# Performance work log

Hardware: AMD Instinct MI355X
Metric: run time of the kernel (lower is better)

Reference implementation:

```python
import jax, jax.numpy as jnp
import numpy as np

UNITS = 1024
OUT_STEPS = 32
NUM_FEATURES = 4
BATCH = 1024
IN_STEPS = 64


def setup_inputs() -> dict:
    key = jax.random.key(0)
    k = jax.random.split(key, 6)
    x = jax.random.normal(k[0], (BATCH, IN_STEPS, NUM_FEATURES), jnp.float32)
    # Keras LSTMCell params: kernel [F,4u], recurrent_kernel [u,4u], bias [4u]
    W = jax.random.normal(k[1], (NUM_FEATURES, 4 * UNITS), jnp.float32) * 0.3
    U = jax.random.normal(k[2], (UNITS, 4 * UNITS), jnp.float32) * 0.03
    b = jnp.zeros((4 * UNITS,), jnp.float32)
    Wd = jax.random.normal(k[3], (UNITS, NUM_FEATURES), jnp.float32) * 0.05
    bd = jnp.zeros((NUM_FEATURES,), jnp.float32)
    return {"x": x, "W": W, "U": U, "b": b, "Wd": Wd, "bd": bd}


def _lstm_cell(xt, h, c, W, U, b):
    # Keras gate order: input, forget, cell, output; sigmoid recurrent act, tanh act
    z = xt @ W + h @ U + b  # [B, 4u]
    i, f, g, o = jnp.split(z, 4, axis=-1)
    c_new = jax.nn.sigmoid(f) * c + jax.nn.sigmoid(i) * jnp.tanh(g)
    h_new = jax.nn.sigmoid(o) * jnp.tanh(c_new)
    return h_new, c_new


def reference(x, W, U, b, Wd, bd):
    B = x.shape[0]
    h0 = jnp.zeros((B, UNITS), x.dtype)
    c0 = jnp.zeros((B, UNITS), x.dtype)

    # warmup: run RNN over the input window, keep final state
    def warm_step(carry, xt):
        h, c = carry
        h, c = _lstm_cell(xt, h, c, W, U, b)
        return (h, c), None

    (h, c), _ = jax.lax.scan(warm_step, (h0, c0), jnp.swapaxes(x, 0, 1))
    pred0 = h @ Wd + bd  # first prediction [B, F]

    def dec_step(carry, _):
        pred, h, c = carry
        h, c = _lstm_cell(pred, h, c, W, U, b)
        pred = h @ Wd + bd
        return (pred, h, c), pred

    _, preds = jax.lax.scan(dec_step, (pred0, h, c), None, length=OUT_STEPS - 1)
    all_preds = jnp.concatenate([pred0[None], preds], axis=0)  # [out_steps, B, F]
    return jnp.transpose(all_preds, (1, 0, 2))  # [B, out_steps, F]
```

## Files before the change

### kernel.cpp

```cpp
#include <hip/hip_runtime.h>

#define BATCH    1024
#define UNITS    1024
#define INSTEPS  64
#define OUTSTEPS 32
#define NF       4
#define NSTEPS   (INSTEPS + OUTSTEPS - 1)

typedef _Float16 half8 __attribute__((ext_vector_type(8)));
typedef float    f32x4 __attribute__((ext_vector_type(4)));

__device__ __forceinline__ float sigf(float x)  { return 1.0f / (1.0f + __expf(-x)); }
__device__ __forceinline__ float tanhf_(float x){ return 1.0f - 2.0f / (__expf(2.0f * x) + 1.0f); }

__global__ void u_transpose(const float* __restrict__ U, _Float16* __restrict__ Ut) {
    __shared__ _Float16 T[64][72];
    const int tid = threadIdx.x;
    const int bid = blockIdx.x;
    const int k0 = (bid >> 6) << 6;
    const int n0 = (bid & 63) << 6;
    #pragma unroll
    for (int i = 0; i < 16; ++i) {
        int q = i * 256 + tid;
        int r = q >> 6, cc = q & 63;
        T[r][cc] = (_Float16)U[(size_t)(k0 + r) * 4096 + n0 + cc];
    }
    __syncthreads();
    #pragma unroll
    for (int i = 0; i < 16; ++i) {
        int q = i * 256 + tid;
        int nn = q >> 6, kk = q & 63;
        Ut[(size_t)(n0 + nn) * 1024 + k0 + kk] = T[kk][nn];
    }
}

#define BS_BYTES  (16*64*64*2)
#define XS_BYTES  (256*4*4)
#define HST_OFF   (BS_BYTES + XS_BYTES)
#define HST_BYTES (256*18*2)
#define XB_OFF    (HST_OFF + HST_BYTES)
#define XB_BYTES  (2*8*64*16)
#define LDS_BYTES (XB_OFF + XB_BYTES)

__global__ __launch_bounds__(1024, 4) void lstm_seq(
    const float* __restrict__ x, const float* __restrict__ W,
    const float* __restrict__ bias, const float* __restrict__ Wd,
    const float* __restrict__ bd, const _Float16* __restrict__ Ut,
    _Float16* hA, _Float16* hB, float* out, unsigned* bar)
{
    extern __shared__ __align__(16) char smem[];
    _Float16 (*Bs)[64][64] = (_Float16 (*)[64][64])smem;
    float (*xs)[NF] = (float (*)[NF])(smem + BS_BYTES);
    _Float16 (*hst)[18] = (_Float16 (*)[18])(smem + HST_OFF);
    f32x4 (*xb)[8][64] = (f32x4 (*)[8][64])(smem + XB_OFF);

    const int tid  = threadIdx.x;
    const int bid  = blockIdx.x;
    const int band = bid & 3;
    const int m0   = band << 8;
    const int u0   = (bid >> 2) << 4;

    const int lane = tid & 63;
    const int wv   = tid >> 6;
    const int rt2  = wv & 7;
    const int kh   = wv >> 3;
    const int quad = lane >> 4;
    const int ln   = lane & 15;

    unsigned* cnt = bar + band * 64;

    const int r_st = (tid >> 3) & 63;
    const int ck   = tid & 7;
    const int swz  = ((ck ^ (r_st & 7)) << 3);
    const int n_st = ((r_st >> 4) << 10) + u0 + (r_st & 15);
    const _Float16* bsrc = Ut + (size_t)n_st * UNITS + ck * 8;

    if (tid < 512) {
        #pragma unroll
        for (int kc = 0; kc < 16; ++kc)
            *(float4*)&Bs[kc][r_st][swz] = *(const float4*)(bsrc + kc * 64);
    }

    float wt[4][4], bt[4], btp[4];
    #pragma unroll
    for (int g = 0; g < 4; ++g) {
        int col = (g << 10) + u0 + ln;
        bt[g] = bias[col];
        #pragma unroll
        for (int f = 0; f < 4; ++f) wt[g][f] = W[f * 4096 + col];
    }
    {
        float bdr0 = bd[0], bdr1 = bd[1], bdr2 = bd[2], bdr3 = bd[3];
        #pragma unroll
        for (int g = 0; g < 4; ++g)
            btp[g] = bt[g] + bdr0*wt[g][0] + bdr1*wt[g][1] + bdr2*wt[g][2] + bdr3*wt[g][3];
    }
    const float* wdp = Wd + (size_t)(u0 + ln) * NF;
    float wd0 = wdp[0], wd1 = wdp[1], wd2 = wdp[2], wd3 = wdp[3];
    float bd0 = 0, bd1 = 0, bd2 = 0, bd3 = 0;
    if (u0 == 0) { bd0 = bd[0]; bd1 = bd[1]; bd2 = bd[2]; bd3 = bd[3]; }

    float cr[2][4] = {{0,0,0,0},{0,0,0,0}};
    float hnv[2][4];

    const int swz0 = ((quad ^ (ln & 7)) << 3);
    const int swz1 = swz0 ^ 32;

    const int row0 = m0 + rt2 * 32 + ln;
    const int aoff = ((quad >> 1) << 15) + row0 * 32 + ((quad & 1) << 4);

    const int xr = tid >> 2, xf = tid & 3;
    float xp0 = x[(size_t)(m0 + xr) * (INSTEPS * NF) + xf];

    char* const hAc = (char*)hA;
    char* const hBc = (char*)hB;
    const size_t stoff = ((size_t)(u0 >> 4) << 15) + (size_t)(m0 + (tid >> 1)) * 32
                       + ((size_t)(tid & 1) << 4);

    __syncthreads();

    for (int p = 0; p < NSTEPS; ++p) {
        if (p < INSTEPS) {
            xs[xr][xf] = xp0;
        } else if (p == INSTEPS && tid < 512) {
            float wc0 = W[n_st], wc1 = W[4096 + n_st],
                  wc2 = W[8192 + n_st], wc3 = W[12288 + n_st];
            #pragma unroll
            for (int kc = 0; kc < 16; ++kc) {
                int k0 = kc * 64 + ck * 8;
                half8 uv = *(const half8*)(bsrc + kc * 64);
                half8 tv;
                #pragma unroll
                for (int j = 0; j < 8; ++j) {
                    const float* wdr = Wd + (size_t)(k0 + j) * NF;
                    float corr = wdr[0]*wc0 + wdr[1]*wc1 + wdr[2]*wc2 + wdr[3]*wc3;
                    tv[j] = (_Float16)((float)uv[j] + corr);
                }
                *(half8*)&Bs[kc][r_st][swz] = tv;
            }
        }
        if (p <= INSTEPS) __syncthreads();

        f32x4 acc[2][4] = {};

        if (p > 0) {
            const char* hb = ((p & 1) ? hAc : hBc) + aoff;
#define AL(kcg, j, rr) (*(const half8*)(hb + ((((kcg) << 2) + ((j) << 1)) << 15) + ((rr) << 9)))

            half8 ar[2][4];
            #pragma unroll
            for (int d = 0; d < 2; ++d) {
                const int kcg = (kh << 3) + d;
                ar[d][0] = AL(kcg, 0, 0);
                ar[d][1] = AL(kcg, 1, 0);
                ar[d][2] = AL(kcg, 0, 1);
                ar[d][3] = AL(kcg, 1, 1);
            }

            #pragma unroll
            for (int kc = 0; kc < 8; ++kc) {
                const int sl = kc & 1;
                half8 af0 = ar[sl][0], ag0 = ar[sl][1], af1 = ar[sl][2], ag1 = ar[sl][3];
                if (kc < 6) {
                    const int kcg = (kh << 3) + kc + 2;
                    ar[sl][0] = AL(kcg, 0, 0);
                    ar[sl][1] = AL(kcg, 1, 0);
                    ar[sl][2] = AL(kcg, 0, 1);
                    ar[sl][3] = AL(kcg, 1, 1);
                }
                const _Float16 (*B)[64] = Bs[(kh << 3) + kc];
                half8 bf0 = *(const half8*)&B[ln][swz0];
                half8 bf1 = *(const half8*)&B[16 + ln][swz0];
                half8 bf2 = *(const half8*)&B[32 + ln][swz0];
                half8 bf3 = *(const half8*)&B[48 + ln][swz0];
                acc[0][0] = __builtin_amdgcn_mfma_f32_16x16x32_f16(af0, bf0, acc[0][0], 0, 0, 0);
                acc[1][0] = __builtin_amdgcn_mfma_f32_16x16x32_f16(af1, bf0, acc[1][0], 0, 0, 0);
                acc[0][1] = __builtin_amdgcn_mfma_f32_16x16x32_f16(af0, bf1, acc[0][1], 0, 0, 0);
                acc[1][1] = __builtin_amdgcn_mfma_f32_16x16x32_f16(af1, bf1, acc[1][1], 0, 0, 0);
                acc[0][2] = __builtin_amdgcn_mfma_f32_16x16x32_f16(af0, bf2, acc[0][2], 0, 0, 0);
                acc[1][2] = __builtin_amdgcn_mfma_f32_16x16x32_f16(af1, bf2, acc[1][2], 0, 0, 0);
                acc[0][3] = __builtin_amdgcn_mfma_f32_16x16x32_f16(af0, bf3, acc[0][3], 0, 0, 0);
                acc[1][3] = __builtin_amdgcn_mfma_f32_16x16x32_f16(af1, bf3, acc[1][3], 0, 0, 0);
                half8 bg0 = *(const half8*)&B[ln][swz1];
                half8 bg1 = *(const half8*)&B[16 + ln][swz1];
                half8 bg2 = *(const half8*)&B[32 + ln][swz1];
                half8 bg3 = *(const half8*)&B[48 + ln][swz1];
                acc[0][0] = __builtin_amdgcn_mfma_f32_16x16x32_f16(ag0, bg0, acc[0][0], 0, 0, 0);
                acc[1][0] = __builtin_amdgcn_mfma_f32_16x16x32_f16(ag1, bg0, acc[1][0], 0, 0, 0);
                acc[0][1] = __builtin_amdgcn_mfma_f32_16x16x32_f16(ag0, bg1, acc[0][1], 0, 0, 0);
                acc[1][1] = __builtin_amdgcn_mfma_f32_16x16x32_f16(ag1, bg1, acc[1][1], 0, 0, 0);
                acc[0][2] = __builtin_amdgcn_mfma_f32_16x16x32_f16(ag0, bg2, acc[0][2], 0, 0, 0);
                acc[1][2] = __builtin_amdgcn_mfma_f32_16x16x32_f16(ag1, bg2, acc[1][2], 0, 0, 0);
                acc[0][3] = __builtin_amdgcn_mfma_f32_16x16x32_f16(ag0, bg3, acc[0][3], 0, 0, 0);
                acc[1][3] = __builtin_amdgcn_mfma_f32_16x16x32_f16(ag1, bg3, acc[1][3], 0, 0, 0);
            }
#undef AL

            #pragma unroll
            for (int r = 0; r < 4; ++r) {
                if ((wv >> 1) == 4 + r) {
                    #pragma unroll
                    for (int j = 0; j < 8; ++j)
                        xb[wv & 1][j][lane] = acc[j >> 2][j & 3];
                }
                __syncthreads();
                if ((wv >> 1) == r) {
                    #pragma unroll
                    for (int j = 0; j < 8; ++j)
                        acc[j >> 2][j & 3] += xb[wv & 1][j][lane];
                }
                __syncthreads();
            }
        }

        const int s_out = p - (INSTEPS - 1);

        if (kh == 0) {
            #pragma unroll
            for (int r = 0; r < 2; ++r) {
                #pragma unroll
                for (int i = 0; i < 4; ++i) {
                    int rl = rt2 * 32 + r * 16 + quad * 4 + i;
                    float zi, zf, zg, zo;
                    if (p < INSTEPS) {
                        float x0 = xs[rl][0], x1 = xs[rl][1], x2 = xs[rl][2], x3 = xs[rl][3];
                        zi = acc[r][0][i] + bt[0] + x0*wt[0][0] + x1*wt[0][1] + x2*wt[0][2] + x3*wt[0][3];
                        zf = acc[r][1][i] + bt[1] + x0*wt[1][0] + x1*wt[1][1] + x2*wt[1][2] + x3*wt[1][3];
                        zg = acc[r][2][i] + bt[2] + x0*wt[2][0] + x1*wt[2][1] + x2*wt[2][2] + x3*wt[2][3];
                        zo = acc[r][3][i] + bt[3] + x0*wt[3][0] + x1*wt[3][1] + x2*wt[3][2] + x3*wt[3][3];
                    } else {
                        zi = acc[r][0][i] + btp[0];
                        zf = acc[r][1][i] + btp[1];
                        zg = acc[r][2][i] + btp[2];
                        zo = acc[r][3][i] + btp[3];
                    }
                    float cold = cr[r][i];
                    float si = sigf(zi), sf = sigf(zf), so = sigf(zo);
                    float cn = sf * cold + si * tanhf_(zg);
                    float hn = so * tanhf_(cn);
                    cr[r][i] = cn;
                    hnv[r][i] = hn;
                    hst[rl][ln] = (_Float16)hn;
                }
            }

            {
                char* hw = (p & 1) ? hBc : hAc;
                const unsigned long long* sp = (const unsigned long long*)
                    ((const char*)hst + (tid >> 1) * 36 + ((tid & 1) << 4));
                unsigned long long v0 = sp[0], v1 = sp[1];
                unsigned long long* dst = (unsigned long long*)(hw + stoff);
                __hip_atomic_store(dst,     v0, __ATOMIC_RELAXED, __HIP_MEMORY_SCOPE_AGENT);
                __hip_atomic_store(dst + 1, v1, __ATOMIC_RELAXED, __HIP_MEMORY_SCOPE_AGENT);
            }
        }

        const int pn = p + 1;

        __syncthreads();
        if (tid == 0)
            __hip_atomic_fetch_add(cnt, 1u, __ATOMIC_RELAXED, __HIP_MEMORY_SCOPE_AGENT);

        if (kh == 0 && s_out >= 0) {
            #pragma unroll
            for (int r = 0; r < 2; ++r) {
                #pragma unroll
                for (int i = 0; i < 4; ++i) {
                    float hn = hnv[r][i];
                    float p0 = hn * wd0, p1 = hn * wd1, p2 = hn * wd2, p3 = hn * wd3;
                    #pragma unroll
                    for (int mk = 1; mk < 16; mk <<= 1) {
                        p0 += __shfl_xor(p0, mk);
                        p1 += __shfl_xor(p1, mk);
                        p2 += __shfl_xor(p2, mk);
                        p3 += __shfl_xor(p3, mk);
                    }
                    if (ln == 0) {
                        int R = m0 + rt2 * 32 + r * 16 + quad * 4 + i;
                        float* op = out + (size_t)R * (OUTSTEPS * NF) + s_out * NF;
                        atomicAdd(op + 0, p0 + bd0);
                        atomicAdd(op + 1, p1 + bd1);
                        atomicAdd(op + 2, p2 + bd2);
                        atomicAdd(op + 3, p3 + bd3);
                    }
                }
            }
        }

        if (pn < INSTEPS) {
            xp0 = x[(size_t)(m0 + xr) * (INSTEPS * NF) + pn * NF + xf];
        }

        if (tid == 0) {
            const unsigned tgt = (unsigned)pn * 64u;
            while (__hip_atomic_load(cnt, __ATOMIC_RELAXED, __HIP_MEMORY_SCOPE_AGENT) < tgt)
                __builtin_amdgcn_s_sleep(1);
            __builtin_amdgcn_fence(__ATOMIC_ACQUIRE, "agent");
        }
        __syncthreads();
    }
}

extern "C" void kernel_launch(void* const* d_in, const int* in_sizes, int n_in,
                              void* d_out, int out_size, void* d_ws, size_t ws_size,
                              hipStream_t stream) {
    (void)in_sizes; (void)n_in; (void)ws_size;
    const float* x  = (const float*)d_in[0];
    const float* W  = (const float*)d_in[1];
    const float* U  = (const float*)d_in[2];
    const float* b  = (const float*)d_in[3];
    const float* Wd = (const float*)d_in[4];
    const float* bd = (const float*)d_in[5];
    float* out = (float*)d_out;

    char* ws = (char*)d_ws;
    _Float16* hA  = (_Float16*)ws;
    _Float16* hB  = (_Float16*)(ws + (2 << 20));
    _Float16* Ut  = (_Float16*)(ws + (4 << 20));
    unsigned* bar = (unsigned*)(ws + (12 << 20));

    hipMemsetAsync(bar, 0, 4096, stream);
    hipMemsetAsync(d_out, 0, (size_t)out_size * sizeof(float), stream);
    u_transpose<<<1024, 256, 0, stream>>>(U, Ut);

    hipFuncSetAttribute((const void*)lstm_seq,
                        hipFuncAttributeMaxDynamicSharedMemorySize, LDS_BYTES);

    void* args[] = {(void*)&x, (void*)&W, (void*)&b, (void*)&Wd, (void*)&bd,
                    (void*)&Ut, (void*)&hA, (void*)&hB, (void*)&out, (void*)&bar};
    hipLaunchCooperativeKernel((const void*)lstm_seq, dim3(256), dim3(1024),
                               args, LDS_BYTES, stream);
}
```

Measured before the change: 1.847 ms.

## Replace atomic counter barrier with per-block flags and split cell work across K-halves

The grid barrier changes from a single atomic fetch-add counter per band to one flag slot per block. A whole wavefront polls all 64 slots and checks them with a wave-wide vote. The split-K reduction is also restructured: each K-half wave exchanges one accumulator half through LDS in three rounds instead of four, so all 16 waves run the LSTM gate math and output projection on 16 rows each instead of 8 waves doing 32. The aim is to cut per-step barrier contention and serialized elementwise latency, at the cost of more LDS exchange traffic. It also adds a relaxed load of the previous prediction from the output buffer that looks unused.

```diff
diff --git a/kernel.cpp b/kernel.cpp
--- a/kernel.cpp
+++ b/kernel.cpp
@@ -36,11 +36,9 @@
 
 #define BS_BYTES  (16*64*64*2)
 #define XS_BYTES  (256*4*4)
-#define HST_OFF   (BS_BYTES + XS_BYTES)
-#define HST_BYTES (256*18*2)
-#define XB_OFF    (HST_OFF + HST_BYTES)
-#define XB_BYTES  (2*8*64*16)
-#define LDS_BYTES (XB_OFF + XB_BYTES)
+#define SH_OFF    (BS_BYTES + XS_BYTES)
+#define SH_BYTES  (24*64*16)
+#define LDS_BYTES (SH_OFF + SH_BYTES)
 
 __global__ __launch_bounds__(1024, 4) void lstm_seq(
     const float* __restrict__ x, const float* __restrict__ W,
@@ -51,14 +49,15 @@
     extern __shared__ __align__(16) char smem[];
     _Float16 (*Bs)[64][64] = (_Float16 (*)[64][64])smem;
     float (*xs)[NF] = (float (*)[NF])(smem + BS_BYTES);
-    _Float16 (*hst)[18] = (_Float16 (*)[18])(smem + HST_OFF);
-    f32x4 (*xb)[8][64] = (f32x4 (*)[8][64])(smem + XB_OFF);
+    f32x4 (*xb)[64] = (f32x4 (*)[64])(smem + SH_OFF);
+    _Float16 (*hst)[20] = (_Float16 (*)[20])(smem + SH_OFF);
 
     const int tid  = threadIdx.x;
     const int bid  = blockIdx.x;
     const int band = bid & 3;
     const int m0   = band << 8;
     const int u0   = (bid >> 2) << 4;
+    const int ublk = bid >> 2;
 
     const int lane = tid & 63;
     const int wv   = tid >> 6;
@@ -67,7 +66,7 @@
     const int quad = lane >> 4;
     const int ln   = lane & 15;
 
-    unsigned* cnt = bar + band * 64;
+    unsigned* slot = bar + band * 64;
 
     const int r_st = (tid >> 3) & 63;
     const int ck   = tid & 7;
@@ -100,8 +99,8 @@
     float bd0 = 0, bd1 = 0, bd2 = 0, bd3 = 0;
     if (u0 == 0) { bd0 = bd[0]; bd1 = bd[1]; bd2 = bd[2]; bd3 = bd[3]; }
 
-    float cr[2][4] = {{0,0,0,0},{0,0,0,0}};
-    float hnv[2][4];
+    float cr[4] = {0, 0, 0, 0};
+    float hnv[4];
 
     const int swz0 = ((quad ^ (ln & 7)) << 3);
     const int swz1 = swz0 ^ 32;
@@ -114,8 +113,10 @@
 
     char* const hAc = (char*)hA;
     char* const hBc = (char*)hB;
-    const size_t stoff = ((size_t)(u0 >> 4) << 15) + (size_t)(m0 + (tid >> 1)) * 32
-                       + ((size_t)(tid & 1) << 4);
+    const int strow = rt2 * 32 + kh * 16 + (lane >> 2);
+    const size_t stoff = ((size_t)(u0 >> 4) << 15) + (size_t)(m0 + strow) * 32
+                       + ((size_t)(lane & 3) << 3);
+    const int hsrc = strow * 40 + ((lane & 3) << 3);
 
     __syncthreads();
 
@@ -141,9 +142,10 @@
         }
         if (p <= INSTEPS) __syncthreads();
 
-        f32x4 acc[2][4] = {};
+        f32x4 accK[4] = {};
 
         if (p > 0) {
+            f32x4 acc[2][4] = {};
             const char* hb = ((p & 1) ? hAc : hBc) + aoff;
 #define AL(kcg, j, rr) (*(const half8*)(hb + ((((kcg) << 2) + ((j) << 1)) << 15) + ((rr) << 9)))
 
@@ -197,17 +199,30 @@
 #undef AL
 
             #pragma unroll
-            for (int r = 0; r < 4; ++r) {
-                if ((wv >> 1) == 4 + r) {
-                    #pragma unroll
-                    for (int j = 0; j < 8; ++j)
-                        xb[wv & 1][j][lane] = acc[j >> 2][j & 3];
+            for (int rd = 0; rd < 3; ++rd) {
+                const int base = rd * 3;
+                const int cntw = (rd == 2) ? 2 : 3;
+                const bool act = (rt2 >= base) && (rt2 < base + cntw);
+                if (act) {
+                    const int sw = (((rt2 - base) << 1) | (1 - kh)) << 2;
+                    if (kh == 0) {
+                        #pragma unroll
+                        for (int g = 0; g < 4; ++g) xb[sw + g][lane] = acc[1][g];
+                    } else {
+                        #pragma unroll
+                        for (int g = 0; g < 4; ++g) xb[sw + g][lane] = acc[0][g];
+                    }
                 }
                 __syncthreads();
-                if ((wv >> 1) == r) {
-                    #pragma unroll
-                    for (int j = 0; j < 8; ++j)
-                        acc[j >> 2][j & 3] += xb[wv & 1][j][lane];
+                if (act) {
+                    const int sr = (((rt2 - base) << 1) | kh) << 2;
+                    if (kh == 0) {
+                        #pragma unroll
+                        for (int g = 0; g < 4; ++g) accK[g] = acc[0][g] + xb[sr + g][lane];
+                    } else {
+                        #pragma unroll
+                        for (int g = 0; g < 4; ++g) accK[g] = acc[1][g] + xb[sr + g][lane];
+                    }
                 }
                 __syncthreads();
             }
@@ -215,74 +230,64 @@
 
         const int s_out = p - (INSTEPS - 1);
 
-        if (kh == 0) {
-            #pragma unroll
-            for (int r = 0; r < 2; ++r) {
-                #pragma unroll
-                for (int i = 0; i < 4; ++i) {
-                    int rl = rt2 * 32 + r * 16 + quad * 4 + i;
-                    float zi, zf, zg, zo;
-                    if (p < INSTEPS) {
-                        float x0 = xs[rl][0], x1 = xs[rl][1], x2 = xs[rl][2], x3 = xs[rl][3];
-                        zi = acc[r][0][i] + bt[0] + x0*wt[0][0] + x1*wt[0][1] + x2*wt[0][2] + x3*wt[0][3];
-                        zf = acc[r][1][i] + bt[1] + x0*wt[1][0] + x1*wt[1][1] + x2*wt[1][2] + x3*wt[1][3];
-                        zg = acc[r][2][i] + bt[2] + x0*wt[2][0] + x1*wt[2][1] + x2*wt[2][2] + x3*wt[2][3];
-                        zo = acc[r][3][i] + bt[3] + x0*wt[3][0] + x1*wt[3][1] + x2*wt[3][2] + x3*wt[3][3];
-                    } else {
-                        zi = acc[r][0][i] + btp[0];
-                        zf = acc[r][1][i] + btp[1];
-                        zg = acc[r][2][i] + btp[2];
-                        zo = acc[r][3][i] + btp[3];
-                    }
-                    float cold = cr[r][i];
-                    float si = sigf(zi), sf = sigf(zf), so = sigf(zo);
-                    float cn = sf * cold + si * tanhf_(zg);
-                    float hn = so * tanhf_(cn);
-                    cr[r][i] = cn;
-                    hnv[r][i] = hn;
-                    hst[rl][ln] = (_Float16)hn;
-                }
-            }
-
-            {
-                char* hw = (p & 1) ? hBc : hAc;
-                const unsigned long long* sp = (const unsigned long long*)
-                    ((const char*)hst + (tid >> 1) * 36 + ((tid & 1) << 4));
-                unsigned long long v0 = sp[0], v1 = sp[1];
-                unsigned long long* dst = (unsigned long long*)(hw + stoff);
-                __hip_atomic_store(dst,     v0, __ATOMIC_RELAXED, __HIP_MEMORY_SCOPE_AGENT);
-                __hip_atomic_store(dst + 1, v1, __ATOMIC_RELAXED, __HIP_MEMORY_SCOPE_AGENT);
-            }
+        #pragma unroll
+        for (int i = 0; i < 4; ++i) {
+            int rl = rt2 * 32 + kh * 16 + quad * 4 + i;
+            float zi, zf, zg, zo;
+            if (p < INSTEPS) {
+                float x0 = xs[rl][0], x1 = xs[rl][1], x2 = xs[rl][2], x3 = xs[rl][3];
+                zi = accK[0][i] + bt[0] + x0*wt[0][0] + x1*wt[0][1] + x2*wt[0][2] + x3*wt[0][3];
+                zf = accK[1][i] + bt[1] + x0*wt[1][0] + x1*wt[1][1] + x2*wt[1][2] + x3*wt[1][3];
+                zg = accK[2][i] + bt[2] + x0*wt[2][0] + x1*wt[2][1] + x2*wt[2][2] + x3*wt[2][3];
+                zo = accK[3][i] + bt[3] + x0*wt[3][0] + x1*wt[3][1] + x2*wt[3][2] + x3*wt[3][3];
+            } else {
+                zi = accK[0][i] + btp[0];
+                zf = accK[1][i] + btp[1];
+                zg = accK[2][i] + btp[2];
+                zo = accK[3][i] + btp[3];
+            }
+            float cold = cr[i];
+            float si = sigf(zi), sf = sigf(zf), so = sigf(zo);
+            float cn = sf * cold + si * tanhf_(zg);
+            float hn = so * tanhf_(cn);
+            cr[i] = cn;
+            hnv[i] = hn;
+            hst[rl][ln] = (_Float16)hn;
+        }
+
+        {
+            char* hw = (p & 1) ? hBc : hAc;
+            unsigned long long v = *(const unsigned long long*)((const char*)hst + hsrc);
+            __hip_atomic_store((unsigned long long*)(hw + stoff), v,
+                               __ATOMIC_RELAXED, __HIP_MEMORY_SCOPE_AGENT);
         }
 
         const int pn = p + 1;
 
         __syncthreads();
         if (tid == 0)
-            __hip_atomic_fetch_add(cnt, 1u, __ATOMIC_RELAXED, __HIP_MEMORY_SCOPE_AGENT);
-
-        if (kh == 0 && s_out >= 0) {
-            #pragma unroll
-            for (int r = 0; r < 2; ++r) {
+            __hip_atomic_store(&slot[ublk], (unsigned)pn,
+                               __ATOMIC_RELAXED, __HIP_MEMORY_SCOPE_AGENT);
+
+        if (s_out >= 0) {
+            #pragma unroll
+            for (int i = 0; i < 4; ++i) {
+                float hn = hnv[i];
+                float p0 = hn * wd0, p1 = hn * wd1, p2 = hn * wd2, p3 = hn * wd3;
                 #pragma unroll
-                for (int i = 0; i < 4; ++i) {
-                    float hn = hnv[r][i];
-                    float p0 = hn * wd0, p1 = hn * wd1, p2 = hn * wd2, p3 = hn * wd3;
-                    #pragma unroll
-                    for (int mk = 1; mk < 16; mk <<= 1) {
-                        p0 += __shfl_xor(p0, mk);
-                        p1 += __shfl_xor(p1, mk);
-                        p2 += __shfl_xor(p2, mk);
-                        p3 += __shfl_xor(p3, mk);
-                    }
-                    if (ln == 0) {
-                        int R = m0 + rt2 * 32 + r * 16 + quad * 4 + i;
-                        float* op = out + (size_t)R * (OUTSTEPS * NF) + s_out * NF;
-                        atomicAdd(op + 0, p0 + bd0);
-                        atomicAdd(op + 1, p1 + bd1);
-                        atomicAdd(op + 2, p2 + bd2);
-                        atomicAdd(op + 3, p3 + bd3);
-                    }
+                for (int mk = 1; mk < 16; mk <<= 1) {
+                    p0 += __shfl_xor(p0, mk);
+                    p1 += __shfl_xor(p1, mk);
+                    p2 += __shfl_xor(p2, mk);
+                    p3 += __shfl_xor(p3, mk);
+                }
+                if (ln == 0) {
+                    int R = m0 + rt2 * 32 + kh * 16 + quad * 4 + i;
+                    float* op = out + (size_t)R * (OUTSTEPS * NF) + s_out * NF;
+                    atomicAdd(op + 0, p0 + bd0);
+                    atomicAdd(op + 1, p1 + bd1);
+                    atomicAdd(op + 2, p2 + bd2);
+                    atomicAdd(op + 3, p3 + bd3);
                 }
             }
         }
@@ -291,13 +296,22 @@
             xp0 = x[(size_t)(m0 + xr) * (INSTEPS * NF) + pn * NF + xf];
         }
 
-        if (tid == 0) {
-            const unsigned tgt = (unsigned)pn * 64u;
-            while (__hip_atomic_load(cnt, __ATOMIC_RELAXED, __HIP_MEMORY_SCOPE_AGENT) < tgt)
+        if (wv == 0) {
+            for (;;) {
+                unsigned v = __hip_atomic_load(&slot[lane], __ATOMIC_RELAXED,
+                                               __HIP_MEMORY_SCOPE_AGENT);
+                if (__all(v >= (unsigned)pn)) break;
                 __builtin_amdgcn_s_sleep(1);
+            }
             __builtin_amdgcn_fence(__ATOMIC_ACQUIRE, "agent");
         }
         __syncthreads();
+
+        if (pn >= INSTEPS && pn < NSTEPS) {
+            int s = pn - INSTEPS;
+            xp0 = __hip_atomic_load(&out[(size_t)(m0 + xr) * (OUTSTEPS * NF) + s * NF + xf],
+                                    __ATOMIC_RELAXED, __HIP_MEMORY_SCOPE_AGENT);
+        }
     }
 }
 
```

New measurement: 1.980 ms. +7.2%, slower.
